# Kernel tuning notes

Measured on AMD Instinct MI355X. Metric: run time of the kernel, lower is better.

## Reference

```python
import jax, jax.numpy as jnp
import numpy as np

N = 50000          # nodes
E = 800000         # edges per metapath
M = 3              # metapaths
IN_DIM = 256
H = 8              # heads
D = 32             # out_dim per head
HID = 128          # semantic attention hidden
NEG_SLOPE = 0.2    # DGL GATConv default leaky_relu slope


def setup_inputs() -> dict:
    key = jax.random.key(0)
    ks = jax.random.split(key, 10)
    h = jax.random.normal(ks[0], (N, IN_DIM), dtype=jnp.float32)
    src = jax.random.randint(ks[1], (M, E), 0, N, dtype=jnp.int32)
    dst = jax.random.randint(ks[2], (M, E), 0, N, dtype=jnp.int32)
    s = 1.0 / np.sqrt(IN_DIM)
    fc_w = jax.random.normal(ks[3], (M, IN_DIM, H * D), dtype=jnp.float32) * s
    attn_l = jax.random.normal(ks[4], (M, H, D), dtype=jnp.float32) * 0.1
    attn_r = jax.random.normal(ks[5], (M, H, D), dtype=jnp.float32) * 0.1
    bias = jnp.zeros((M, H * D), dtype=jnp.float32)
    sem_w1 = jax.random.normal(ks[6], (H * D, HID), dtype=jnp.float32) * (1.0 / np.sqrt(H * D))
    sem_b1 = jnp.zeros((HID,), dtype=jnp.float32)
    sem_w2 = jax.random.normal(ks[7], (HID, 1), dtype=jnp.float32) * (1.0 / np.sqrt(HID))
    return {"h": h, "src": src, "dst": dst, "fc_w": fc_w, "attn_l": attn_l,
            "attn_r": attn_r, "bias": bias, "sem_w1": sem_w1, "sem_b1": sem_b1,
            "sem_w2": sem_w2}


def _gat(h, src, dst, fc_w, attn_l, attn_r, bias):
    # DGL GATConv (eval mode, dropout=0), activation=elu.
    feat = (h @ fc_w).reshape(N, H, D)                       # [N,H,D]
    el = jnp.sum(feat * attn_l, axis=-1)                     # [N,H]
    er = jnp.sum(feat * attn_r, axis=-1)                     # [N,H]
    e = jax.nn.leaky_relu(el[src] + er[dst], NEG_SLOPE)      # [E,H]
    # edge softmax over incoming edges of each dst node
    emax = jax.ops.segment_max(e, dst, num_segments=N)       # [N,H]
    emax = jnp.where(jnp.isfinite(emax), emax, 0.0)
    ee = jnp.exp(e - emax[dst])                              # [E,H]
    esum = jax.ops.segment_sum(ee, dst, num_segments=N)      # [N,H]
    alpha = ee / jnp.maximum(esum[dst], 1e-38)               # [E,H]
    msg = feat[src] * alpha[:, :, None]                      # [E,H,D]
    rst = jax.ops.segment_sum(msg, dst, num_segments=N)      # [N,H,D]
    rst = rst + bias.reshape(1, H, D)
    return jax.nn.elu(rst).reshape(N, H * D)                 # flatten heads


def reference(h, src, dst, fc_w, attn_l, attn_r, bias, sem_w1, sem_b1, sem_w2):
    gat_all = jax.vmap(_gat, in_axes=(None, 0, 0, 0, 0, 0, 0))
    z_m = gat_all(h, src, dst, fc_w, attn_l, attn_r, bias)   # [M,N,F]
    z_m = jnp.transpose(z_m, (1, 0, 2))                      # [N,M,F]
    # semantic attention
    w = jnp.tanh(z_m @ sem_w1 + sem_b1) @ sem_w2             # [N,M,1]
    w = w.mean(axis=0)                                       # [M,1]
    a_w = jax.nn.softmax(w, axis=0)                          # [M,1]
    z = jnp.sum(z_m * a_w[None, :, :], axis=1)               # [N,F]
    return z
```

## Files before the change

### kernel.cpp

```cpp
#include <hip/hip_runtime.h>
#include <math.h>

#define NN   50000
#define EE   800000
#define MM   3
#define KDIM 256
#define FF   256
#define HH   8
#define DD   32
#define HID  128
#define SLOPE 0.2f
#define BK   32
#define CAP  80

typedef unsigned short u16;
typedef unsigned int   u32;
typedef __attribute__((ext_vector_type(8))) short short8;
typedef __attribute__((ext_vector_type(4))) float floatx4;

__device__ __forceinline__ float eluf(float x) { return x > 0.f ? x : expm1f(x); }

__device__ __forceinline__ float b2f_lo(u32 u) {
    union { u32 i; float f; } v; v.i = u << 16; return v.f;
}
__device__ __forceinline__ float b2f_hi(u32 u) {
    union { u32 i; float f; } v; v.i = u & 0xffff0000u; return v.f;
}
__device__ __forceinline__ u16 f2b(float f) {
    union { float f; u32 i; } v; v.f = f;
    u32 lsb = (v.i >> 16) & 1u;
    v.i += 0x7fffu + lsb;
    return (u16)(v.i >> 16);
}
__device__ __forceinline__ u32 pack2(float lo, float hi) {
    return (u32)f2b(lo) | ((u32)f2b(hi) << 16);
}

__device__ __forceinline__ void gload_lds16(const u16* g, u16* l) {
    __builtin_amdgcn_global_load_lds(
        (const __attribute__((address_space(1))) unsigned int*)(const void*)g,
        (__attribute__((address_space(3))) unsigned int*)(void*)l,
        16, 0, 0);
}

__global__ __launch_bounds__(256) void k_cast_h(
    const float* __restrict__ hmat, u16* __restrict__ hb)
{
    long long i = ((long long)blockIdx.x * 256 + threadIdx.x) * 8;
    if (i >= (long long)NN * KDIM) return;
    float4 v0 = *(const float4*)(hmat + i);
    float4 v1 = *(const float4*)(hmat + i + 4);
    uint4 u;
    u.x = pack2(v0.x, v0.y); u.y = pack2(v0.z, v0.w);
    u.z = pack2(v1.x, v1.y); u.w = pack2(v1.z, v1.w);
    *(uint4*)(hb + i) = u;
}

__global__ __launch_bounds__(256) void k_cast_w(
    const float* __restrict__ fcw, u16* __restrict__ fcwt)
{
    int k = blockIdx.x, m = blockIdx.y, n = threadIdx.x;
    float v = fcw[((size_t)m * KDIM + k) * FF + n];
    fcwt[((size_t)m * FF + n) * KDIM + k] = f2b(v);
}

__global__ __launch_bounds__(128) void k_cast_w1(
    const float* __restrict__ w1, u16* __restrict__ w1t)
{
    int k = blockIdx.x, n = threadIdx.x;
    w1t[(size_t)n * KDIM + k] = f2b(w1[(size_t)k * HID + n]);
}

__global__ __launch_bounds__(256) void k_scatter_fixed(
    const int* __restrict__ src, const int* __restrict__ dst,
    int* __restrict__ cnt, u16* __restrict__ srt)
{
    int e = blockIdx.x * 256 + threadIdx.x;
    int m = blockIdx.y;
    if (e < EE) {
        size_t eg = (size_t)m * EE + e;
        int d = dst[eg];
        int slot = atomicAdd(&cnt[(size_t)m * NN + d], 1);
        if (slot < CAP) srt[(size_t)(m * CAP + slot) * NN + d] = (u16)src[eg];
    }
}

__global__ __launch_bounds__(256) void k_feat_all(
    const u16*   __restrict__ hb,
    const u16*   __restrict__ fcwt,
    const float* __restrict__ al,
    const float* __restrict__ ar,
    u16*   __restrict__ featb,
    float* __restrict__ el,
    float* __restrict__ er)
{
    __shared__ u16 As[128 * BK];
    __shared__ u16 Bs[128 * BK];

    const int n0 = blockIdx.x * 128;
    const int cy = blockIdx.y;
    const int m  = blockIdx.z;
    const int c_base = cy * 128;
    const int t = threadIdx.x;
    const int wave = t >> 6, lane = t & 63;
    const int wr = wave >> 1, wc = wave & 1;
    const int quad = lane >> 4, l15 = lane & 15;

    const u16* fcwt_m = fcwt + (size_t)m * FF * KDIM;
    const float* al_m = al + (size_t)m * HH * DD;
    const float* ar_m = ar + (size_t)m * HH * DD;

    const u16* pA[2]; const u16* pB[2]; u16* lA[2]; u16* lB[2];
    #pragma unroll
    for (int i = 0; i < 2; ++i) {
        int r  = wave * 32 + i * 16 + (lane >> 2);
        int cs = (((lane & 3) ^ (r & 3)) << 3);
        pA[i] = hb + (size_t)min(n0 + r, NN - 1) * KDIM + cs;
        pB[i] = fcwt_m + (size_t)(c_base + r) * KDIM + cs;
        lA[i] = (u16*)As + (wave * 2 + i) * 512;
        lB[i] = (u16*)Bs + (wave * 2 + i) * 512;
    }

    int aoff[4], boff[4];
    #pragma unroll
    for (int ti = 0; ti < 4; ++ti) {
        int rowa = wr * 64 + ti * 16 + l15;
        aoff[ti] = rowa * BK + (((quad ^ (rowa & 3))) << 3);
        int rowb = wc * 64 + ti * 16 + l15;
        boff[ti] = rowb * BK + (((quad ^ (rowb & 3))) << 3);
    }

    floatx4 acc[4][4] = {};

    for (int k0 = 0; k0 < KDIM; k0 += BK) {
        __syncthreads();
        #pragma unroll
        for (int i = 0; i < 2; ++i) {
            gload_lds16(pA[i] + k0, lA[i]);
            gload_lds16(pB[i] + k0, lB[i]);
        }
        __syncthreads();

        short8 afr[4], bfr[4];
        #pragma unroll
        for (int ti = 0; ti < 4; ++ti)
            afr[ti] = *(const short8*)(&As[aoff[ti]]);
        #pragma unroll
        for (int tj = 0; tj < 4; ++tj)
            bfr[tj] = *(const short8*)(&Bs[boff[tj]]);
        #pragma unroll
        for (int ti = 0; ti < 4; ++ti)
            #pragma unroll
            for (int tj = 0; tj < 4; ++tj)
                acc[ti][tj] = __builtin_amdgcn_mfma_f32_16x16x32_bf16(
                    afr[ti], bfr[tj], acc[ti][tj], 0, 0, 0);
    }

    float alv[4], arv[4];
    #pragma unroll
    for (int tj = 0; tj < 4; ++tj) {
        int h = cy * 4 + wc * 2 + (tj >> 1);
        int dcol = (tj & 1) * 16 + l15;
        alv[tj] = al_m[h * DD + dcol];
        arv[tj] = ar_m[h * DD + dcol];
    }
    const int h0 = cy * 4 + wc * 2, h1 = h0 + 1;

    #pragma unroll
    for (int ti = 0; ti < 4; ++ti) {
        #pragma unroll
        for (int reg = 0; reg < 4; ++reg) {
            int n = n0 + wr * 64 + ti * 16 + quad * 4 + reg;
            bool ok = n < NN;
            if (ok) {
                #pragma unroll
                for (int tj = 0; tj < 4; ++tj) {
                    int c = c_base + wc * 64 + tj * 16 + l15;
                    featb[((size_t)m * NN + n) * FF + c] = f2b(acc[ti][tj][reg]);
                }
            }
            float pl0 = acc[ti][0][reg] * alv[0] + acc[ti][1][reg] * alv[1];
            float pl1 = acc[ti][2][reg] * alv[2] + acc[ti][3][reg] * alv[3];
            float pr0 = acc[ti][0][reg] * arv[0] + acc[ti][1][reg] * arv[1];
            float pr1 = acc[ti][2][reg] * arv[2] + acc[ti][3][reg] * arv[3];
            #pragma unroll
            for (int s = 1; s < 16; s <<= 1) {
                pl0 += __shfl_xor(pl0, s); pl1 += __shfl_xor(pl1, s);
                pr0 += __shfl_xor(pr0, s); pr1 += __shfl_xor(pr1, s);
            }
            if (l15 == 0 && ok) {
                el[((size_t)m * NN + n) * HH + h0] = pl0;
                el[((size_t)m * NN + n) * HH + h1] = pl1;
                er[((size_t)m * NN + n) * HH + h0] = pr0;
                er[((size_t)m * NN + n) * HH + h1] = pr1;
            }
        }
    }
}

__global__ __launch_bounds__(256) void k_aggr_all(
    const int* __restrict__ cnt,
    const u16* __restrict__ srt,
    const float* __restrict__ el,
    const float* __restrict__ er,
    const u16* __restrict__ featb,
    const float* __restrict__ bias,
    u16* __restrict__ z)
{
    __shared__ float alpha_s[4][2][CAP][HH];
    __shared__ int   srcoff[4][2][CAP];

    const int m = blockIdx.y;
    const int wave = threadIdx.x >> 6, lane = threadIdx.x & 63;
    const int half = lane >> 5, L = lane & 31;
    const int d = blockIdx.x * 8 + wave * 2 + half;

    const int deg = min(cnt[(size_t)m * NN + d], CAP);
    const float* el_m = el + (size_t)m * NN * HH;
    const u16* feat_m = featb + (size_t)m * NN * FF;

    #pragma unroll
    for (int i = 0; i < 3; ++i) {
        int slot = L + i * 32;
        if (slot < deg)
            srcoff[wave][half][slot] =
                (int)srt[(size_t)(m * CAP + slot) * NN + d] * FF;
    }

    const int hA = L & 7;
    const float er_d = er[((size_t)m * NN + d) * HH + hA];
    float esum_r = 0.f;
    const int nIter = (deg + 3) >> 2;
    int i = 0;
    for (; i + 2 <= nIter; i += 2) {
        int j0 = i * 4 + (L >> 3);
        int j1 = j0 + 4;
        bool v0 = j0 < deg, v1 = j1 < deg;
        int so0 = v0 ? srcoff[wave][half][j0] : 0;
        int so1 = v1 ? srcoff[wave][half][j1] : 0;
        float x0 = el_m[(size_t)(so0 >> 5) + hA] + er_d;
        float x1 = el_m[(size_t)(so1 >> 5) + hA] + er_d;
        x0 = x0 >= 0.f ? x0 : SLOPE * x0;  x0 = fminf(x0, 60.f);
        x1 = x1 >= 0.f ? x1 : SLOPE * x1;  x1 = fminf(x1, 60.f);
        float e0 = v0 ? expf(x0) : 0.f;
        float e1 = v1 ? expf(x1) : 0.f;
        if (v0) alpha_s[wave][half][j0][hA] = e0;
        if (v1) alpha_s[wave][half][j1][hA] = e1;
        float g = e0 + e1;
        g += __shfl_xor(g, 8); g += __shfl_xor(g, 16);
        esum_r += g;
    }
    for (; i < nIter; ++i) {
        int j = i * 4 + (L >> 3);
        float e = 0.f;
        if (j < deg) {
            int so = srcoff[wave][half][j];
            float x = el_m[(size_t)(so >> 5) + hA] + er_d;
            x = x >= 0.f ? x : SLOPE * x;
            x = fminf(x, 60.f);
            e = expf(x);
            alpha_s[wave][half][j][hA] = e;
        }
        float g = e;
        g += __shfl_xor(g, 8); g += __shfl_xor(g, 16);
        esum_r += g;
    }
    float inv_r = 1.f / fmaxf(esum_r, 1e-38f);

    const float inv_g = __shfl(inv_r, (lane & 32) | (L >> 2));
    const int hB = L >> 2;
    const u16* frow = feat_m + L * 8;
    float acc[8] = {0.f, 0.f, 0.f, 0.f, 0.f, 0.f, 0.f, 0.f};

#define ACC8(f, a)                                                  \
    acc[0] += (a) * b2f_lo((f).x); acc[1] += (a) * b2f_hi((f).x);   \
    acc[2] += (a) * b2f_lo((f).y); acc[3] += (a) * b2f_hi((f).y);   \
    acc[4] += (a) * b2f_lo((f).z); acc[5] += (a) * b2f_hi((f).z);   \
    acc[6] += (a) * b2f_lo((f).w); acc[7] += (a) * b2f_hi((f).w);

    int j = 0;
    for (; j + 4 <= deg; j += 4) {
        int so0 = srcoff[wave][half][j + 0];
        int so1 = srcoff[wave][half][j + 1];
        int so2 = srcoff[wave][half][j + 2];
        int so3 = srcoff[wave][half][j + 3];
        float a0 = alpha_s[wave][half][j + 0][hB];
        float a1 = alpha_s[wave][half][j + 1][hB];
        float a2 = alpha_s[wave][half][j + 2][hB];
        float a3 = alpha_s[wave][half][j + 3][hB];
        uint4 f0 = *(const uint4*)(frow + so0);
        uint4 f1 = *(const uint4*)(frow + so1);
        uint4 f2 = *(const uint4*)(frow + so2);
        uint4 f3 = *(const uint4*)(frow + so3);
        ACC8(f0, a0); ACC8(f1, a1); ACC8(f2, a2); ACC8(f3, a3);
    }
    for (; j < deg; ++j) {
        int so = srcoff[wave][half][j];
        float a = alpha_s[wave][half][j][hB];
        uint4 f = *(const uint4*)(frow + so);
        ACC8(f, a);
    }
#undef ACC8

    #pragma unroll
    for (int k = 0; k < 8; ++k) acc[k] *= inv_g;

    const float4 b0 = *(const float4*)(bias + (size_t)m * FF + L * 8);
    const float4 b1 = *(const float4*)(bias + (size_t)m * FF + L * 8 + 4);
    uint4 o;
    o.x = pack2(eluf(acc[0] + b0.x), eluf(acc[1] + b0.y));
    o.y = pack2(eluf(acc[2] + b0.z), eluf(acc[3] + b0.w));
    o.z = pack2(eluf(acc[4] + b1.x), eluf(acc[5] + b1.y));
    o.w = pack2(eluf(acc[6] + b1.z), eluf(acc[7] + b1.w));
    *(uint4*)(z + ((size_t)m * NN + d) * FF + L * 8) = o;
}

__global__ __launch_bounds__(256) void k_sem_all(
    const u16* __restrict__ z,
    const u16* __restrict__ w1t,
    const float* __restrict__ b1,
    const float* __restrict__ w2,
    float* __restrict__ wsum)
{
    __shared__ u16 As[128 * BK];
    __shared__ u16 Bs[128 * BK];

    const int n0 = blockIdx.x * 128;
    const int m  = blockIdx.y;
    const int t = threadIdx.x;
    const int wave = t >> 6, lane = t & 63;
    const int wr = wave >> 1, wc = wave & 1;
    const int quad = lane >> 4, l15 = lane & 15;

    const u16* z_m = z + (size_t)m * NN * FF;

    const u16* pA[2]; const u16* pB[2]; u16* lA[2]; u16* lB[2];
    #pragma unroll
    for (int i = 0; i < 2; ++i) {
        int r  = wave * 32 + i * 16 + (lane >> 2);
        int cs = (((lane & 3) ^ (r & 3)) << 3);
        pA[i] = z_m + (size_t)min(n0 + r, NN - 1) * FF + cs;
        pB[i] = w1t + (size_t)r * KDIM + cs;
        lA[i] = (u16*)As + (wave * 2 + i) * 512;
        lB[i] = (u16*)Bs + (wave * 2 + i) * 512;
    }

    int aoff[4], boff[4];
    #pragma unroll
    for (int ti = 0; ti < 4; ++ti) {
        int rowa = wr * 64 + ti * 16 + l15;
        aoff[ti] = rowa * BK + (((quad ^ (rowa & 3))) << 3);
        int rowb = wc * 64 + ti * 16 + l15;
        boff[ti] = rowb * BK + (((quad ^ (rowb & 3))) << 3);
    }

    floatx4 acc[4][4] = {};

    for (int k0 = 0; k0 < KDIM; k0 += BK) {
        __syncthreads();
        #pragma unroll
        for (int i = 0; i < 2; ++i) {
            gload_lds16(pA[i] + k0, lA[i]);
            gload_lds16(pB[i] + k0, lB[i]);
        }
        __syncthreads();

        short8 afr[4], bfr[4];
        #pragma unroll
        for (int ti = 0; ti < 4; ++ti)
            afr[ti] = *(const short8*)(&As[aoff[ti]]);
        #pragma unroll
        for (int tj = 0; tj < 4; ++tj)
            bfr[tj] = *(const short8*)(&Bs[boff[tj]]);
        #pragma unroll
        for (int ti = 0; ti < 4; ++ti)
            #pragma unroll
            for (int tj = 0; tj < 4; ++tj)
                acc[ti][tj] = __builtin_amdgcn_mfma_f32_16x16x32_bf16(
                    afr[ti], bfr[tj], acc[ti][tj], 0, 0, 0);
    }

    float b1v[4], w2v[4];
    #pragma unroll
    for (int tj = 0; tj < 4; ++tj) {
        int c = wc * 64 + tj * 16 + l15;
        b1v[tj] = b1[c];
        w2v[tj] = w2[c];
    }
    float local = 0.f;
    #pragma unroll
    for (int ti = 0; ti < 4; ++ti) {
        #pragma unroll
        for (int reg = 0; reg < 4; ++reg) {
            int n = n0 + wr * 64 + ti * 16 + quad * 4 + reg;
            if (n < NN) {
                #pragma unroll
                for (int tj = 0; tj < 4; ++tj)
                    local += tanhf(acc[ti][tj][reg] + b1v[tj]) * w2v[tj];
            }
        }
    }
    #pragma unroll
    for (int s = 1; s < 64; s <<= 1) local += __shfl_xor(local, s);
    if (lane == 0) atomicAdd(&wsum[m], local);
}

__global__ __launch_bounds__(256) void k_combine(
    const u16* __restrict__ z, const float* __restrict__ wsum,
    float* __restrict__ out)
{
    float s0 = wsum[0] / (float)NN, s1 = wsum[1] / (float)NN, s2 = wsum[2] / (float)NN;
    float mx = fmaxf(s0, fmaxf(s1, s2));
    float e0 = expf(s0 - mx), e1 = expf(s1 - mx), e2 = expf(s2 - mx);
    float inv = 1.f / (e0 + e1 + e2);
    float aw[3] = { e0 * inv, e1 * inv, e2 * inv };

    long long idx = (long long)blockIdx.x * 256 + threadIdx.x;
    if (idx >= (long long)NN * 32) return;
    int n = (int)(idx >> 5), c = (int)(idx & 31) * 8;
    float acc[8] = {0.f, 0.f, 0.f, 0.f, 0.f, 0.f, 0.f, 0.f};
    #pragma unroll
    for (int m = 0; m < MM; ++m) {
        uint4 f = *(const uint4*)(z + ((size_t)m * NN + n) * FF + c);
        float a = aw[m];
        acc[0] += a * b2f_lo(f.x); acc[1] += a * b2f_hi(f.x);
        acc[2] += a * b2f_lo(f.y); acc[3] += a * b2f_hi(f.y);
        acc[4] += a * b2f_lo(f.z); acc[5] += a * b2f_hi(f.z);
        acc[6] += a * b2f_lo(f.w); acc[7] += a * b2f_hi(f.w);
    }
    float* op = out + (size_t)n * FF + c;
    *(float4*)op       = make_float4(acc[0], acc[1], acc[2], acc[3]);
    *(float4*)(op + 4) = make_float4(acc[4], acc[5], acc[6], acc[7]);
}

extern "C" void kernel_launch(void* const* d_in, const int* in_sizes, int n_in,
                              void* d_out, int out_size, void* d_ws, size_t ws_size,
                              hipStream_t stream)
{
    const float* hmat = (const float*)d_in[0];
    const int*   src  = (const int*)d_in[1];
    const int*   dst  = (const int*)d_in[2];
    const float* fcw  = (const float*)d_in[3];
    const float* al   = (const float*)d_in[4];
    const float* ar   = (const float*)d_in[5];
    const float* bias = (const float*)d_in[6];
    const float* w1   = (const float*)d_in[7];
    const float* b1   = (const float*)d_in[8];
    const float* w2   = (const float*)d_in[9];
    float* out = (float*)d_out;

    char* ws = (char*)d_ws;
    size_t off = 0;
    auto alloc = [&](size_t nbytes) {
        void* p = (void*)(ws + off);
        off = (off + nbytes + 255) & ~(size_t)255;
        return p;
    };
    float* el   = (float*)alloc((size_t)MM * NN * HH * 4);
    float* er   = (float*)alloc((size_t)MM * NN * HH * 4);
    float* wsum = (float*)alloc(256);
    int*   cnt  = (int*)alloc((size_t)MM * NN * 4);
    u16*   srt  = (u16*)alloc((size_t)MM * CAP * NN * 2);
    u16*   fcwt = (u16*)alloc((size_t)MM * KDIM * FF * 2);
    u16*   w1t  = (u16*)alloc((size_t)HID * KDIM * 2);
    u16*   hb   = (u16*)alloc((size_t)NN * KDIM * 2);
    u16*   featb= (u16*)alloc((size_t)MM * NN * FF * 2);
    u16*   z    = (u16*)alloc((size_t)MM * NN * FF * 2);

    hipMemsetAsync(wsum, 0, 256, stream);
    hipMemsetAsync(cnt, 0, (size_t)MM * NN * 4, stream);

    k_cast_h<<<(int)(((size_t)NN * KDIM / 8 + 255) / 256), 256, 0, stream>>>(hmat, hb);
    k_cast_w<<<dim3(KDIM, MM), 256, 0, stream>>>(fcw, fcwt);
    k_cast_w1<<<KDIM, 128, 0, stream>>>(w1, w1t);

    k_scatter_fixed<<<dim3((EE + 255) / 256, MM), 256, 0, stream>>>(src, dst, cnt, srt);

    k_feat_all<<<dim3((NN + 127) / 128, 2, MM), 256, 0, stream>>>(
        hb, fcwt, al, ar, featb, el, er);
    k_aggr_all<<<dim3(NN / 8, MM), 256, 0, stream>>>(cnt, srt, el, er, featb, bias, z);
    k_sem_all<<<dim3((NN + 127) / 128, MM), 256, 0, stream>>>(z, w1t, b1, w2, wsum);
    k_combine<<<(int)(((size_t)NN * 32 + 255) / 256), 256, 0, stream>>>(z, wsum, out);
}
```

Measured before the change: 605.5 us.

## Double-buffer LDS tiles in GEMM kernels and split aggregation launches

Both bf16 MFMA GEMM kernels (feature projection and semantic attention) now use two LDS buffers, so the next K-tile is loaded while the current one is multiplied, and one barrier per iteration replaces two. Separately, the aggregation kernel is launched six times, once per metapath and half of the nodes, instead of as a single 2D grid, likely to improve cache locality of the feature gather. Double buffering doubles LDS use per block, which may lower occupancy. The extra launches add launch overhead.

```diff
diff --git a/kernel.cpp b/kernel.cpp
--- a/kernel.cpp
+++ b/kernel.cpp
@@ -94,8 +94,8 @@
     float* __restrict__ el,
     float* __restrict__ er)
 {
-    __shared__ u16 As[128 * BK];
-    __shared__ u16 Bs[128 * BK];
+    __shared__ u16 As[2][128 * BK];
+    __shared__ u16 Bs[2][128 * BK];
 
     const int n0 = blockIdx.x * 128;
     const int cy = blockIdx.y;
@@ -110,15 +110,14 @@
     const float* al_m = al + (size_t)m * HH * DD;
     const float* ar_m = ar + (size_t)m * HH * DD;
 
-    const u16* pA[2]; const u16* pB[2]; u16* lA[2]; u16* lB[2];
+    const u16* pA[2]; const u16* pB[2]; int lo[2];
     #pragma unroll
     for (int i = 0; i < 2; ++i) {
         int r  = wave * 32 + i * 16 + (lane >> 2);
         int cs = (((lane & 3) ^ (r & 3)) << 3);
         pA[i] = hb + (size_t)min(n0 + r, NN - 1) * KDIM + cs;
         pB[i] = fcwt_m + (size_t)(c_base + r) * KDIM + cs;
-        lA[i] = (u16*)As + (wave * 2 + i) * 512;
-        lB[i] = (u16*)Bs + (wave * 2 + i) * 512;
+        lo[i] = (wave * 2 + i) * 512;
     }
 
     int aoff[4], boff[4];
@@ -132,28 +131,38 @@
 
     floatx4 acc[4][4] = {};
 
+    #pragma unroll
+    for (int i = 0; i < 2; ++i) {
+        gload_lds16(pA[i], &As[0][lo[i]]);
+        gload_lds16(pB[i], &Bs[0][lo[i]]);
+    }
+    __syncthreads();
+
+    int cur = 0;
     for (int k0 = 0; k0 < KDIM; k0 += BK) {
-        __syncthreads();
-        #pragma unroll
-        for (int i = 0; i < 2; ++i) {
-            gload_lds16(pA[i] + k0, lA[i]);
-            gload_lds16(pB[i] + k0, lB[i]);
+        int nxt = cur ^ 1;
+        if (k0 + BK < KDIM) {
+            #pragma unroll
+            for (int i = 0; i < 2; ++i) {
+                gload_lds16(pA[i] + k0 + BK, &As[nxt][lo[i]]);
+                gload_lds16(pB[i] + k0 + BK, &Bs[nxt][lo[i]]);
+            }
         }
-        __syncthreads();
-
         short8 afr[4], bfr[4];
         #pragma unroll
         for (int ti = 0; ti < 4; ++ti)
-            afr[ti] = *(const short8*)(&As[aoff[ti]]);
+            afr[ti] = *(const short8*)(&As[cur][aoff[ti]]);
         #pragma unroll
         for (int tj = 0; tj < 4; ++tj)
-            bfr[tj] = *(const short8*)(&Bs[boff[tj]]);
+            bfr[tj] = *(const short8*)(&Bs[cur][boff[tj]]);
         #pragma unroll
         for (int ti = 0; ti < 4; ++ti)
             #pragma unroll
             for (int tj = 0; tj < 4; ++tj)
                 acc[ti][tj] = __builtin_amdgcn_mfma_f32_16x16x32_bf16(
                     afr[ti], bfr[tj], acc[ti][tj], 0, 0, 0);
+        __syncthreads();
+        cur = nxt;
     }
 
     float alv[4], arv[4];
@@ -205,15 +214,15 @@
     const float* __restrict__ er,
     const u16* __restrict__ featb,
     const float* __restrict__ bias,
-    u16* __restrict__ z)
+    u16* __restrict__ z,
+    int m, int d_base)
 {
     __shared__ float alpha_s[4][2][CAP][HH];
     __shared__ int   srcoff[4][2][CAP];
 
-    const int m = blockIdx.y;
     const int wave = threadIdx.x >> 6, lane = threadIdx.x & 63;
     const int half = lane >> 5, L = lane & 31;
-    const int d = blockIdx.x * 8 + wave * 2 + half;
+    const int d = d_base + blockIdx.x * 8 + wave * 2 + half;
 
     const int deg = min(cnt[(size_t)m * NN + d], CAP);
     const float* el_m = el + (size_t)m * NN * HH;
@@ -322,8 +331,8 @@
     const float* __restrict__ w2,
     float* __restrict__ wsum)
 {
-    __shared__ u16 As[128 * BK];
-    __shared__ u16 Bs[128 * BK];
+    __shared__ u16 As[2][128 * BK];
+    __shared__ u16 Bs[2][128 * BK];
 
     const int n0 = blockIdx.x * 128;
     const int m  = blockIdx.y;
@@ -334,15 +343,14 @@
 
     const u16* z_m = z + (size_t)m * NN * FF;
 
-    const u16* pA[2]; const u16* pB[2]; u16* lA[2]; u16* lB[2];
+    const u16* pA[2]; const u16* pB[2]; int lo[2];
     #pragma unroll
     for (int i = 0; i < 2; ++i) {
         int r  = wave * 32 + i * 16 + (lane >> 2);
         int cs = (((lane & 3) ^ (r & 3)) << 3);
         pA[i] = z_m + (size_t)min(n0 + r, NN - 1) * FF + cs;
         pB[i] = w1t + (size_t)r * KDIM + cs;
-        lA[i] = (u16*)As + (wave * 2 + i) * 512;
-        lB[i] = (u16*)Bs + (wave * 2 + i) * 512;
+        lo[i] = (wave * 2 + i) * 512;
     }
 
     int aoff[4], boff[4];
@@ -356,28 +364,38 @@
 
     floatx4 acc[4][4] = {};
 
+    #pragma unroll
+    for (int i = 0; i < 2; ++i) {
+        gload_lds16(pA[i], &As[0][lo[i]]);
+        gload_lds16(pB[i], &Bs[0][lo[i]]);
+    }
+    __syncthreads();
+
+    int cur = 0;
     for (int k0 = 0; k0 < KDIM; k0 += BK) {
-        __syncthreads();
-        #pragma unroll
-        for (int i = 0; i < 2; ++i) {
-            gload_lds16(pA[i] + k0, lA[i]);
-            gload_lds16(pB[i] + k0, lB[i]);
+        int nxt = cur ^ 1;
+        if (k0 + BK < KDIM) {
+            #pragma unroll
+            for (int i = 0; i < 2; ++i) {
+                gload_lds16(pA[i] + k0 + BK, &As[nxt][lo[i]]);
+                gload_lds16(pB[i] + k0 + BK, &Bs[nxt][lo[i]]);
+            }
         }
-        __syncthreads();
-
         short8 afr[4], bfr[4];
         #pragma unroll
         for (int ti = 0; ti < 4; ++ti)
-            afr[ti] = *(const short8*)(&As[aoff[ti]]);
+            afr[ti] = *(const short8*)(&As[cur][aoff[ti]]);
         #pragma unroll
         for (int tj = 0; tj < 4; ++tj)
-            bfr[tj] = *(const short8*)(&Bs[boff[tj]]);
+            bfr[tj] = *(const short8*)(&Bs[cur][boff[tj]]);
         #pragma unroll
         for (int ti = 0; ti < 4; ++ti)
             #pragma unroll
             for (int tj = 0; tj < 4; ++tj)
                 acc[ti][tj] = __builtin_amdgcn_mfma_f32_16x16x32_bf16(
                     afr[ti], bfr[tj], acc[ti][tj], 0, 0, 0);
+        __syncthreads();
+        cur = nxt;
     }
 
     float b1v[4], w2v[4];
@@ -478,7 +496,12 @@
 
     k_feat_all<<<dim3((NN + 127) / 128, 2, MM), 256, 0, stream>>>(
         hb, fcwt, al, ar, featb, el, er);
-    k_aggr_all<<<dim3(NN / 8, MM), 256, 0, stream>>>(cnt, srt, el, er, featb, bias, z);
+
+    for (int m = 0; m < MM; ++m)
+        for (int hlf = 0; hlf < 2; ++hlf)
+            k_aggr_all<<<NN / 16, 256, 0, stream>>>(
+                cnt, srt, el, er, featb, bias, z, m, hlf * (NN / 2));
+
     k_sem_all<<<dim3((NN + 127) / 128, MM), 256, 0, stream>>>(z, w1t, b1, w2, wsum);
     k_combine<<<(int)(((size_t)NN * 32 + 255) / 256), 256, 0, stream>>>(z, wsum, out);
 }
```

After: 640.3 us. +5.7%, slower.
